# Optimization experiments

Hardware: AMD Instinct MI355X
Metric: run time of the kernel (lower is better)

## Reference

```python
import jax, jax.numpy as jnp
import numpy as np
from jax import lax

B, C, H, W = 8, 128, 96, 96
EXPAN = 4           # expan_att_chans
NUM_CHANS = 2
NUM_HEADS = NUM_CHANS * EXPAN          # 8
HEAD_DIM = C * EXPAN // NUM_HEADS      # 64
EPS = 1e-12  # F.normalize eps


def _gconv(x, w, b, groups):
    # torch Conv2d(kernel=3, padding=1, groups=groups), OIHW weight layout
    y = lax.conv_general_dilated(x, w, (1, 1), 'SAME',
                                 feature_group_count=groups,
                                 dimension_numbers=('NCHW', 'OIHW', 'NCHW'))
    return y + b[None, :, None, None]


def setup_inputs() -> dict:
    key = jax.random.key(0)
    k0, k1, k2 = jax.random.split(key, 3)
    x = jax.random.normal(k0, (B, C, H, W), jnp.float32)
    w_qkv = jax.random.normal(k1, (C * EXPAN * 3, 1, 3, 3), jnp.float32) * 0.05
    b_qkv = jnp.zeros((C * EXPAN * 3,), jnp.float32)
    t = jnp.ones((1, NUM_HEADS, 1, 1), jnp.float32)
    w_fus = jax.random.normal(k2, (C, EXPAN, 3, 3), jnp.float32) * 0.05
    b_fus = jnp.zeros((C,), jnp.float32)
    return {"x": x, "w_qkv": w_qkv, "b_qkv": b_qkv, "t": t,
            "w_fus": w_fus, "b_fus": b_fus}


def reference(x, w_qkv, b_qkv, t, w_fus, b_fus):
    # depthwise-grouped qkv conv: [B, C*EXPAN*3, H, W]
    qkv = _gconv(x, w_qkv, b_qkv, C)
    # view(B, C, 3e, H, W).transpose(1,2) -> [B, 3e, C, H, W]
    qkv = qkv.reshape(B, C, 3 * EXPAN, H, W).transpose(0, 2, 1, 3, 4)
    q, k, v = jnp.split(qkv, 3, axis=1)  # each [B, EXPAN, C, H, W]

    def heads(a):
        return a.reshape(B, NUM_HEADS, HEAD_DIM, H * W)

    q, k, v = heads(q), heads(k), heads(v)

    def l2n(a):
        return a / jnp.maximum(jnp.linalg.norm(a, axis=-1, keepdims=True), EPS)

    q, k = l2n(q), l2n(k)
    attn = jnp.einsum('bhdn,bhen->bhde', q, k) * t   # [B, nh, hd, hd]
    attn = jax.nn.softmax(attn, axis=-1)
    o = jnp.einsum('bhde,bhen->bhdn', attn, v)       # [B, nh, hd, HW]
    # view(B, EXPAN, C, H, W).transpose(1,2).flatten(1,2) -> [B, C*EXPAN, H, W]
    o = o.reshape(B, EXPAN, C, H, W).transpose(0, 2, 1, 3, 4).reshape(B, C * EXPAN, H, W)
    return _gconv(o, w_fus, b_fus, C)
```

## Files before the change

kernel.cpp:

```cpp
#include <hip/hip_runtime.h>
#include <hip/hip_bf16.h>
#include <stdint.h>

#define BB     8
#define CC     128
#define HW     9216
#define NHEAD  8
#define HD     64
#define NCH    16
#define CHUNK  576
#define KPAD   68
#define VTPAD  68

typedef __hip_bfloat16 bf16;
using frag16 = __attribute__((ext_vector_type(8))) short;
using f32x4  = __attribute__((ext_vector_type(4))) float;

__device__ __forceinline__ float b2f(bf16 v) { return __bfloat162float(v); }
__device__ __forceinline__ bf16  f2b(float v) { return __float2bfloat16(v); }

__device__ __forceinline__ float lo2f(unsigned int u) {
  union { unsigned int i; float f; } c; c.i = u << 16; return c.f;
}
__device__ __forceinline__ float hi2f(unsigned int u) {
  union { unsigned int i; float f; } c; c.i = u & 0xffff0000u; return c.f;
}

__device__ __forceinline__ unsigned int pack2(float a, float b) {
  union { __hip_bfloat162 h2; unsigned int u; } c;
  c.h2 = __float22bfloat162_rn(make_float2(a, b));
  return c.u;
}

__device__ __forceinline__ frag16 ldsfrag(const unsigned short* p) {
  uint2 lo = *(const uint2*)p;
  uint2 hi = *(const uint2*)(p + 4);
  union { unsigned int u[4]; frag16 f; } c;
  c.u[0] = lo.x; c.u[1] = lo.y; c.u[2] = hi.x; c.u[3] = hi.y;
  return c.f;
}
__device__ __forceinline__ void ldsst(unsigned short* p, uint4 v) {
  *(uint2*)p = make_uint2(v.x, v.y);
  *(uint2*)(p + 4) = make_uint2(v.z, v.w);
}

__device__ __forceinline__ void stage_plane(float* xs, const float* xp, int tid) {
  const float4 z4 = make_float4(0.f, 0.f, 0.f, 0.f);
  for (int i = tid; i < 98; i += 256) *(float4*)&xs[i * 100] = z4;
  for (int i = tid; i < 24; i += 256) *(float4*)&xs[4 + i * 4] = z4;
  for (int i = tid; i < 25; i += 256) *(float4*)&xs[9704 + i * 4] = z4;
  for (int i = tid; i < 96 * 24; i += 256) {
    int y = i / 24, g4 = i - y * 24;
    ((float4*)(xs + (y + 1) * 100 + 4))[g4] = ((const float4*)(xp + y * 96))[g4];
  }
}

__global__ __launch_bounds__(256) void k1_qkv(
    const float* __restrict__ x, const float* __restrict__ wq,
    const float* __restrict__ bq,
    bf16* __restrict__ qg, bf16* __restrict__ kg, bf16* __restrict__ vg,
    float* __restrict__ qn2, float* __restrict__ kn2, int b_base) {
  __shared__ float xs[98 * 100 + 4];
  __shared__ float red[32];
  int tid = threadIdx.x;
  int wave = tid >> 6, lane = tid & 63;
  int b = b_base + (blockIdx.x >> 7), c = blockIdx.x & 127;
  const float* xp = x + (size_t)(b * CC + c) * HW;
  stage_plane(xs, xp, tid);
  __syncthreads();

  int half = c >> 6, d = c & 63;
  int nidx[8];
  size_t basep[12];
#pragma unroll
  for (int j = 0; j < 12; ++j) {
    int e = j & 3;
    int h = e * 2 + half;
    int ni = (b * NHEAD + h) * HD + d;
    if (j < 8) nidx[j] = ni;
    basep[j] = (size_t)ni * HW;
  }
  const float* wrow = wq + c * 108;
  const float* brow = bq + c * 12;

  float ssq[8];
#pragma unroll
  for (int j = 0; j < 8; ++j) ssq[j] = 0.f;

#pragma unroll 1
  for (int it = 0; it < 5; ++it) {
    int u = it * 256 + tid;
    if (u < 1152) {
      int ly = u / 12;
      int x8 = (u - ly * 12) * 8;
      int p0 = ly * 96 + x8;
      float w10[3][10];
#pragma unroll
      for (int ky = 0; ky < 3; ++ky) {
        int basea = (ly + ky) * 100 + 4 + x8;
        float4 M0 = *(const float4*)&xs[basea];
        float4 M1 = *(const float4*)&xs[basea + 4];
        w10[ky][0] = xs[basea - 1];
        w10[ky][1] = M0.x; w10[ky][2] = M0.y; w10[ky][3] = M0.z; w10[ky][4] = M0.w;
        w10[ky][5] = M1.x; w10[ky][6] = M1.y; w10[ky][7] = M1.z; w10[ky][8] = M1.w;
        w10[ky][9] = xs[basea + 8];
      }
#pragma unroll
      for (int j = 0; j < 12; ++j) {
        float bias = brow[j];
        float a[8];
#pragma unroll
        for (int p = 0; p < 8; ++p) a[p] = bias;
#pragma unroll
        for (int ky = 0; ky < 3; ++ky)
#pragma unroll
          for (int kx = 0; kx < 3; ++kx) {
            float w = wrow[j * 9 + ky * 3 + kx];
#pragma unroll
            for (int p = 0; p < 8; ++p)
              a[p] = fmaf(w, w10[ky][kx + p], a[p]);
          }
        uint4 st;
        st.x = pack2(a[0], a[1]); st.y = pack2(a[2], a[3]);
        st.z = pack2(a[4], a[5]); st.w = pack2(a[6], a[7]);
        if (j < 4)      *(uint4*)(qg + basep[j] + p0) = st;
        else if (j < 8) *(uint4*)(kg + basep[j] + p0) = st;
        else            *(uint4*)(vg + basep[j] + p0) = st;
        if (j < 8) {
          float s2 = 0.f;
#pragma unroll
          for (int p = 0; p < 8; ++p) s2 = fmaf(a[p], a[p], s2);
          ssq[j] += s2;
        }
      }
    }
  }
#pragma unroll
  for (int j = 0; j < 8; ++j) {
    float v = ssq[j];
#pragma unroll
    for (int off = 32; off > 0; off >>= 1) v += __shfl_down(v, off);
    if (lane == 0) red[wave * 8 + j] = v;
  }
  __syncthreads();
  if (tid < 8) {
    float s = red[tid] + red[8 + tid] + red[16 + tid] + red[24 + tid];
    if (tid < 4) qn2[nidx[tid]] = s;
    else         kn2[nidx[tid]] = s;
  }
}

__global__ __launch_bounds__(256) void k2_gram(
    const bf16* __restrict__ qg, const bf16* __restrict__ kg,
    float* __restrict__ part) {
  __shared__ unsigned short sq[2][64 * KPAD];
  __shared__ unsigned short sk[2][64 * KPAD];
  int tid = threadIdx.x;
  int wave = tid >> 6;
  int lane = tid & 63;
  int chunk = blockIdx.x;
  int bh = blockIdx.y;
  const size_t base = (size_t)bh * HD * HW;
  int n0 = chunk * CHUNK;

  int srow = tid >> 3;
  int sseg = tid & 7;
  const bf16* qs0 = qg + base + (size_t)srow * HW + n0 + sseg * 8;
  const bf16* qs1 = qs0 + (size_t)32 * HW;
  const bf16* ks0 = kg + base + (size_t)srow * HW + n0 + sseg * 8;
  const bf16* ks1 = ks0 + (size_t)32 * HW;
  int d0 = srow * KPAD + sseg * 8;
  int d1 = (srow + 32) * KPAD + sseg * 8;

  int m = lane & 15;
  int k8 = lane >> 4;
  int arow = wave * 16 + m;

  f32x4 acc0 = {0.f, 0.f, 0.f, 0.f}, acc1 = acc0, acc2 = acc0, acc3 = acc0;

  uint4 rq0 = *(const uint4*)(qs0);
  uint4 rq1 = *(const uint4*)(qs1);
  uint4 rk0 = *(const uint4*)(ks0);
  uint4 rk1 = *(const uint4*)(ks1);
  ldsst(&sq[0][d0], rq0); ldsst(&sq[0][d1], rq1);
  ldsst(&sk[0][d0], rk0); ldsst(&sk[0][d1], rk1);
  __syncthreads();

#pragma unroll 1
  for (int s = 0; s < 9; ++s) {
    if (s < 8) {
      int off = (s + 1) * 64;
      rq0 = *(const uint4*)(qs0 + off);
      rq1 = *(const uint4*)(qs1 + off);
      rk0 = *(const uint4*)(ks0 + off);
      rk1 = *(const uint4*)(ks1 + off);
    }
    const unsigned short* sqc = sq[s & 1];
    const unsigned short* skc = sk[s & 1];
#pragma unroll
    for (int kk = 0; kk < 2; ++kk) {
      int co = kk * 32 + k8 * 8;
      frag16 a  = ldsfrag(&sqc[arow * KPAD + co]);
      frag16 b0 = ldsfrag(&skc[(m +  0) * KPAD + co]);
      frag16 b1 = ldsfrag(&skc[(m + 16) * KPAD + co]);
      frag16 b2 = ldsfrag(&skc[(m + 32) * KPAD + co]);
      frag16 b3 = ldsfrag(&skc[(m + 48) * KPAD + co]);
      acc0 = __builtin_amdgcn_mfma_f32_16x16x32_bf16(a, b0, acc0, 0, 0, 0);
      acc1 = __builtin_amdgcn_mfma_f32_16x16x32_bf16(a, b1, acc1, 0, 0, 0);
      acc2 = __builtin_amdgcn_mfma_f32_16x16x32_bf16(a, b2, acc2, 0, 0, 0);
      acc3 = __builtin_amdgcn_mfma_f32_16x16x32_bf16(a, b3, acc3, 0, 0, 0);
    }
    if (s < 8) {
      int nb = (s + 1) & 1;
      ldsst(&sq[nb][d0], rq0); ldsst(&sq[nb][d1], rq1);
      ldsst(&sk[nb][d0], rk0); ldsst(&sk[nb][d1], rk1);
      __syncthreads();
    }
  }

  float* po = part + (size_t)(bh * NCH + chunk) * 4096;
  int dr = wave * 16 + (lane >> 4) * 4;
  int e0 = lane & 15;
#pragma unroll
  for (int r = 0; r < 4; ++r) {
    po[(dr + r) * 64 +  0 + e0] = acc0[r];
    po[(dr + r) * 64 + 16 + e0] = acc1[r];
    po[(dr + r) * 64 + 32 + e0] = acc2[r];
    po[(dr + r) * 64 + 48 + e0] = acc3[r];
  }
}

__global__ __launch_bounds__(256) void k2_softmax(
    const float* __restrict__ part, bf16* __restrict__ ah, bf16* __restrict__ al,
    const float* __restrict__ qn2, const float* __restrict__ kn2,
    const float* __restrict__ t_f) {
  __shared__ float kns[64];
  int bh = blockIdx.x;
  int dq = blockIdx.y;
  int tid = threadIdx.x;
  if (tid < 64) kns[tid] = fmaxf(sqrtf(kn2[bh * 64 + tid]), 1e-12f);
  __syncthreads();
  int d  = dq * 16 + (tid >> 4);
  int e0 = (tid & 15) * 4;

  const float* pb = part + (size_t)bh * NCH * 4096 + d * 64 + e0;
  float4 s = make_float4(0.f, 0.f, 0.f, 0.f);
#pragma unroll
  for (int ch = 0; ch < NCH; ++ch) {
    float4 g = *(const float4*)&pb[ch * 4096];
    s.x += g.x; s.y += g.y; s.z += g.z; s.w += g.w;
  }
  float v[4] = {s.x, s.y, s.z, s.w};
  float sc = t_f[bh & 7] / fmaxf(sqrtf(qn2[bh * 64 + d]), 1e-12f);
  float m = -1e30f;
#pragma unroll
  for (int j = 0; j < 4; ++j) {
    v[j] = v[j] * sc / kns[e0 + j];
    m = fmaxf(m, v[j]);
  }
  m = fmaxf(m, __shfl_xor(m, 1));
  m = fmaxf(m, __shfl_xor(m, 2));
  m = fmaxf(m, __shfl_xor(m, 4));
  m = fmaxf(m, __shfl_xor(m, 8));
  float ssum = 0.f;
#pragma unroll
  for (int j = 0; j < 4; ++j) { v[j] = __expf(v[j] - m); ssum += v[j]; }
  ssum += __shfl_xor(ssum, 1);
  ssum += __shfl_xor(ssum, 2);
  ssum += __shfl_xor(ssum, 4);
  ssum += __shfl_xor(ssum, 8);
  float inv = 1.f / ssum;
  unsigned short hi16[4], lo16[4];
#pragma unroll
  for (int j = 0; j < 4; ++j) {
    float p = v[j] * inv;
    bf16 hi = f2b(p);
    float lo = p - b2f(hi);
    bf16 lov = f2b(lo);
    hi16[j] = *(unsigned short*)&hi;
    lo16[j] = *(unsigned short*)&lov;
  }
  const size_t base = (size_t)bh * 4096 + d * 64 + e0;
  *(ushort4*)(ah + base) = *(ushort4*)&hi16[0];
  *(ushort4*)(al + base) = *(ushort4*)&lo16[0];
}

__global__ __launch_bounds__(256) void k3_av(
    const bf16* __restrict__ ah, const bf16* __restrict__ al,
    const bf16* __restrict__ vg, bf16* __restrict__ og) {
  __shared__ unsigned short vt[256 * VTPAD];
  int tid = threadIdx.x;
  int wave = tid >> 6, lane = tid & 63;
  int chunk = blockIdx.x;
  int bh = blockIdx.y;
  int b = bh >> 3, h = bh & 7;
  int n0 = chunk * 256;
  int m = lane & 15;
  int k8 = (lane >> 4) * 8;
  int nwbase = wave * 64;

  const bf16* vp0 = vg + (size_t)bh * HD * HW + n0;
#pragma unroll
  for (int it = 0; it < 4; ++it) {
    int u = it * 256 + tid;
    int eq = u & 15, nq = u >> 4;
    const bf16* src = vp0 + (size_t)(eq * 4) * HW + nq * 4;
    ushort4 r0 = *(const ushort4*)(src);
    ushort4 r1 = *(const ushort4*)(src + HW);
    ushort4 r2 = *(const ushort4*)(src + 2 * HW);
    ushort4 r3 = *(const ushort4*)(src + (size_t)3 * HW);
    unsigned short* dst = &vt[(nq * 4) * VTPAD + eq * 4];
    *(ushort4*)(dst)             = make_ushort4(r0.x, r1.x, r2.x, r3.x);
    *(ushort4*)(dst + VTPAD)     = make_ushort4(r0.y, r1.y, r2.y, r3.y);
    *(ushort4*)(dst + 2 * VTPAD) = make_ushort4(r0.z, r1.z, r2.z, r3.z);
    *(ushort4*)(dst + 3 * VTPAD) = make_ushort4(r0.w, r1.w, r2.w, r3.w);
  }
  __syncthreads();

  const bf16* ahp = ah + (size_t)bh * 4096;
  const bf16* alp = al + (size_t)bh * 4096;

  f32x4 acc[4][4];
#pragma unroll
  for (int dt = 0; dt < 4; ++dt)
#pragma unroll
    for (int nt = 0; nt < 4; ++nt) acc[dt][nt] = {0.f, 0.f, 0.f, 0.f};

#pragma unroll
  for (int dt = 0; dt < 4; ++dt) {
    frag16 ahf[2], alf[2];
#pragma unroll
    for (int kh = 0; kh < 2; ++kh) {
      ahf[kh] = *(const frag16*)(ahp + (dt * 16 + m) * 64 + kh * 32 + k8);
      alf[kh] = *(const frag16*)(alp + (dt * 16 + m) * 64 + kh * 32 + k8);
    }
#pragma unroll
    for (int nt = 0; nt < 4; ++nt) {
      int nl = nwbase + nt * 16 + m;
#pragma unroll
      for (int kh = 0; kh < 2; ++kh) {
        frag16 bf = ldsfrag(&vt[nl * VTPAD + kh * 32 + k8]);
        acc[dt][nt] = __builtin_amdgcn_mfma_f32_16x16x32_bf16(ahf[kh], bf, acc[dt][nt], 0, 0, 0);
        acc[dt][nt] = __builtin_amdgcn_mfma_f32_16x16x32_bf16(alf[kh], bf, acc[dt][nt], 0, 0, 0);
      }
    }
  }

  int cc0 = (h & 1) * 256 + (h >> 1);
  bf16* ob = og + (size_t)b * 512 * HW;
  int q4 = (lane >> 4) * 4;
#pragma unroll
  for (int dt = 0; dt < 4; ++dt)
#pragma unroll
    for (int nt = 0; nt < 4; ++nt) {
      int n = n0 + nwbase + nt * 16 + m;
#pragma unroll
      for (int r = 0; r < 4; ++r) {
        int d = dt * 16 + q4 + r;
        ob[(size_t)(cc0 + d * 4) * HW + n] = f2b(acc[dt][nt][r]);
      }
    }
}

__global__ __launch_bounds__(256) void k4_fuse(
    const bf16* __restrict__ og, const float* __restrict__ wf,
    const float* __restrict__ bfu, float* __restrict__ out) {
  __shared__ unsigned short cells[26 * 100 * 4];
  int tid = threadIdx.x;
  int tile = blockIdx.x;
  int bc = blockIdx.y;
  int b = bc >> 7, c = bc & 127;
  int r0 = tile * 24 - 1;
  const uint2 z2 = make_uint2(0u, 0u);
  for (int i = tid; i < 52; i += 256) {
    int rr = i >> 1, cc = (i & 1) ? 98 : 1;
    *(uint2*)&cells[(rr * 100 + cc) * 4] = z2;
  }
  const uint4 z4 = make_uint4(0u, 0u, 0u, 0u);
  if (r0 < 0)
    for (int i = tid; i < 48; i += 256) *(uint4*)&cells[(0 * 100 + 2 + i * 2) * 4] = z4;
  if (r0 + 25 >= 96)
    for (int i = tid; i < 48; i += 256) *(uint4*)&cells[(25 * 100 + 2 + i * 2) * 4] = z4;
  const bf16* op = og + (size_t)(b * 512 + c * 4) * HW;
  for (int u = tid; u < 26 * 48; u += 256) {
    int rr = u / 48, pr = u - rr * 48;
    int gr = r0 + rr;
    if (gr >= 0 && gr < 96) {
      int gp = gr * 96 + pr * 2;
      unsigned int A = *(const unsigned int*)(op + gp);
      unsigned int B = *(const unsigned int*)(op + HW + gp);
      unsigned int C = *(const unsigned int*)(op + 2 * HW + gp);
      unsigned int D = *(const unsigned int*)(op + (size_t)3 * HW + gp);
      uint4 w;
      w.x = (A & 0xffffu) | (B << 16);
      w.y = (C & 0xffffu) | (D << 16);
      w.z = (A >> 16) | (B & 0xffff0000u);
      w.w = (C >> 16) | (D & 0xffff0000u);
      *(uint4*)&cells[(rr * 100 + 2 + pr * 2) * 4] = w;
    }
  }
  __syncthreads();
  const float* wrow = wf + c * 36;
  float bias = bfu[c];
  float* outp = out + (size_t)(b * CC + c) * HW + tile * 24 * 96;
#pragma unroll
  for (int pi = 0; pi < 9; ++pi) {
    int p = pi * 256 + tid;
    int ry = p / 96, x = p - ry * 96;
    float a0 = bias, a1 = 0.f, a2 = 0.f, a3 = 0.f;
#pragma unroll
    for (int ky = 0; ky < 3; ++ky) {
      int basec = (ry + ky) * 100 + 1 + x;
#pragma unroll
      for (int kx = 0; kx < 3; ++kx) {
        uint2 cc2 = *(const uint2*)&cells[(basec + kx) * 4];
        a0 = fmaf(wrow[0 + ky * 3 + kx],  lo2f(cc2.x), a0);
        a1 = fmaf(wrow[9 + ky * 3 + kx],  hi2f(cc2.x), a1);
        a2 = fmaf(wrow[18 + ky * 3 + kx], lo2f(cc2.y), a2);
        a3 = fmaf(wrow[27 + ky * 3 + kx], hi2f(cc2.y), a3);
      }
    }
    outp[p] = (a0 + a1) + (a2 + a3);
  }
}

extern "C" void kernel_launch(void* const* d_in, const int* in_sizes, int n_in,
                              void* d_out, int out_size, void* d_ws, size_t ws_size,
                              hipStream_t stream) {
  (void)in_sizes; (void)n_in; (void)out_size; (void)ws_size;
  const float* x   = (const float*)d_in[0];
  const float* wq  = (const float*)d_in[1];
  const float* bq  = (const float*)d_in[2];
  const float* tt  = (const float*)d_in[3];
  const float* wf  = (const float*)d_in[4];
  const float* bfu = (const float*)d_in[5];

  char* ws = (char*)d_ws;
  bf16*  qg    = (bf16*)(ws + 0);
  bf16*  kg    = (bf16*)(ws + 75497472);
  bf16*  vg    = (bf16*)(ws + 150994944);
  float* part  = (float*)(ws + 226492416);
  bf16*  ah    = (bf16*)(ws + 243269632);
  bf16*  al    = (bf16*)(ws + 243793920);
  float* qn2   = (float*)(ws + 244318208);
  float* kn2   = (float*)(ws + 244334592);
  bf16*  og    = qg;
  float* out   = (float*)d_out;

  hipLaunchKernelGGL(k1_qkv, dim3(512), dim3(256), 0, stream,
                     x, wq, bq, qg, kg, vg, qn2, kn2, 0);
  hipLaunchKernelGGL(k1_qkv, dim3(512), dim3(256), 0, stream,
                     x, wq, bq, qg, kg, vg, qn2, kn2, 4);
  hipLaunchKernelGGL(k2_gram, dim3(NCH, 64), dim3(256), 0, stream, qg, kg, part);
  hipLaunchKernelGGL(k2_softmax, dim3(64, 4), dim3(256), 0, stream,
                     part, ah, al, qn2, kn2, tt);
  hipLaunchKernelGGL(k3_av, dim3(36, 64), dim3(256), 0, stream, ah, al, vg, og);
  hipLaunchKernelGGL(k4_fuse, dim3(4, 1024), dim3(256), 0, stream, og, wf, bfu, out);
}
```

Before: 251.8 us.

## Double-chunk AV kernel with prefetched V, swapped MFMA operands, merged qkv launch

```diff
diff --git a/kernel.cpp b/kernel.cpp
--- a/kernel.cpp
+++ b/kernel.cpp
@@ -59,12 +59,12 @@
     const float* __restrict__ x, const float* __restrict__ wq,
     const float* __restrict__ bq,
     bf16* __restrict__ qg, bf16* __restrict__ kg, bf16* __restrict__ vg,
-    float* __restrict__ qn2, float* __restrict__ kn2, int b_base) {
+    float* __restrict__ qn2, float* __restrict__ kn2) {
   __shared__ float xs[98 * 100 + 4];
   __shared__ float red[32];
   int tid = threadIdx.x;
   int wave = tid >> 6, lane = tid & 63;
-  int b = b_base + (blockIdx.x >> 7), c = blockIdx.x & 127;
+  int b = blockIdx.x >> 7, c = blockIdx.x & 127;
   const float* xp = x + (size_t)(b * CC + c) * HW;
   stage_plane(xs, xp, tid);
   __syncthreads();
@@ -291,20 +291,34 @@
   __shared__ unsigned short vt[256 * VTPAD];
   int tid = threadIdx.x;
   int wave = tid >> 6, lane = tid & 63;
-  int chunk = blockIdx.x;
+  int cx = blockIdx.x;
   int bh = blockIdx.y;
   int b = bh >> 3, h = bh & 7;
-  int n0 = chunk * 256;
+  int n0 = cx * 512;
   int m = lane & 15;
   int k8 = (lane >> 4) * 8;
   int nwbase = wave * 64;
 
-  const bf16* vp0 = vg + (size_t)bh * HD * HW + n0;
+  const bf16* ahp = ah + (size_t)bh * 4096;
+  const bf16* alp = al + (size_t)bh * 4096;
+  frag16 b_hi[4][2], b_lo[4][2];
+#pragma unroll
+  for (int dt = 0; dt < 4; ++dt)
+#pragma unroll
+    for (int kh = 0; kh < 2; ++kh) {
+      b_hi[dt][kh] = *(const frag16*)(ahp + (dt * 16 + m) * 64 + kh * 32 + k8);
+      b_lo[dt][kh] = *(const frag16*)(alp + (dt * 16 + m) * 64 + kh * 32 + k8);
+    }
+
+  int ueq = tid & 15, unq = tid >> 4;
+  (void)ueq; (void)unq;
+  const bf16* vbase = vg + (size_t)bh * HD * HW;
+
 #pragma unroll
   for (int it = 0; it < 4; ++it) {
     int u = it * 256 + tid;
     int eq = u & 15, nq = u >> 4;
-    const bf16* src = vp0 + (size_t)(eq * 4) * HW + nq * 4;
+    const bf16* src = vbase + n0 + (size_t)(eq * 4) * HW + nq * 4;
     ushort4 r0 = *(const ushort4*)(src);
     ushort4 r1 = *(const ushort4*)(src + HW);
     ushort4 r2 = *(const ushort4*)(src + 2 * HW);
@@ -317,49 +331,71 @@
   }
   __syncthreads();
 
-  const bf16* ahp = ah + (size_t)bh * 4096;
-  const bf16* alp = al + (size_t)bh * 4096;
-
-  f32x4 acc[4][4];
-#pragma unroll
-  for (int dt = 0; dt < 4; ++dt)
-#pragma unroll
-    for (int nt = 0; nt < 4; ++nt) acc[dt][nt] = {0.f, 0.f, 0.f, 0.f};
-
-#pragma unroll
-  for (int dt = 0; dt < 4; ++dt) {
-    frag16 ahf[2], alf[2];
-#pragma unroll
-    for (int kh = 0; kh < 2; ++kh) {
-      ahf[kh] = *(const frag16*)(ahp + (dt * 16 + m) * 64 + kh * 32 + k8);
-      alf[kh] = *(const frag16*)(alp + (dt * 16 + m) * 64 + kh * 32 + k8);
-    }
-#pragma unroll
-    for (int nt = 0; nt < 4; ++nt) {
-      int nl = nwbase + nt * 16 + m;
-#pragma unroll
-      for (int kh = 0; kh < 2; ++kh) {
-        frag16 bf = ldsfrag(&vt[nl * VTPAD + kh * 32 + k8]);
-        acc[dt][nt] = __builtin_amdgcn_mfma_f32_16x16x32_bf16(ahf[kh], bf, acc[dt][nt], 0, 0, 0);
-        acc[dt][nt] = __builtin_amdgcn_mfma_f32_16x16x32_bf16(alf[kh], bf, acc[dt][nt], 0, 0, 0);
-      }
-    }
-  }
-
   int cc0 = (h & 1) * 256 + (h >> 1);
   bf16* ob = og + (size_t)b * 512 * HW;
   int q4 = (lane >> 4) * 4;
-#pragma unroll
-  for (int dt = 0; dt < 4; ++dt)
+
+  ushort4 pf[4][4];
+
+#pragma unroll 1
+  for (int s = 0; s < 2; ++s) {
+    if (s == 0) {
+#pragma unroll
+      for (int it = 0; it < 4; ++it) {
+        int u = it * 256 + tid;
+        int eq = u & 15, nq = u >> 4;
+        const bf16* src = vbase + n0 + 256 + (size_t)(eq * 4) * HW + nq * 4;
+        pf[it][0] = *(const ushort4*)(src);
+        pf[it][1] = *(const ushort4*)(src + HW);
+        pf[it][2] = *(const ushort4*)(src + 2 * HW);
+        pf[it][3] = *(const ushort4*)(src + (size_t)3 * HW);
+      }
+    }
+    f32x4 acc[4][4];
+#pragma unroll
+    for (int nt = 0; nt < 4; ++nt)
+#pragma unroll
+      for (int dt = 0; dt < 4; ++dt) acc[nt][dt] = {0.f, 0.f, 0.f, 0.f};
+
 #pragma unroll
     for (int nt = 0; nt < 4; ++nt) {
-      int n = n0 + nwbase + nt * 16 + m;
-#pragma unroll
-      for (int r = 0; r < 4; ++r) {
-        int d = dt * 16 + q4 + r;
-        ob[(size_t)(cc0 + d * 4) * HW + n] = f2b(acc[dt][nt][r]);
-      }
-    }
+      int nl = nwbase + nt * 16 + m;
+      frag16 af0 = ldsfrag(&vt[nl * VTPAD + 0 + k8]);
+      frag16 af1 = ldsfrag(&vt[nl * VTPAD + 32 + k8]);
+#pragma unroll
+      for (int dt = 0; dt < 4; ++dt) {
+        acc[nt][dt] = __builtin_amdgcn_mfma_f32_16x16x32_bf16(af0, b_hi[dt][0], acc[nt][dt], 0, 0, 0);
+        acc[nt][dt] = __builtin_amdgcn_mfma_f32_16x16x32_bf16(af0, b_lo[dt][0], acc[nt][dt], 0, 0, 0);
+        acc[nt][dt] = __builtin_amdgcn_mfma_f32_16x16x32_bf16(af1, b_hi[dt][1], acc[nt][dt], 0, 0, 0);
+        acc[nt][dt] = __builtin_amdgcn_mfma_f32_16x16x32_bf16(af1, b_lo[dt][1], acc[nt][dt], 0, 0, 0);
+      }
+    }
+    int ns0 = n0 + s * 256 + nwbase + q4;
+#pragma unroll
+    for (int nt = 0; nt < 4; ++nt)
+#pragma unroll
+      for (int dt = 0; dt < 4; ++dt) {
+        int d = dt * 16 + m;
+        uint2 st = make_uint2(pack2(acc[nt][dt][0], acc[nt][dt][1]),
+                              pack2(acc[nt][dt][2], acc[nt][dt][3]));
+        *(uint2*)(ob + (size_t)(cc0 + d * 4) * HW + ns0 + nt * 16) = st;
+      }
+    if (s == 0) {
+      __syncthreads();
+#pragma unroll
+      for (int it = 0; it < 4; ++it) {
+        int u = it * 256 + tid;
+        int eq = u & 15, nq = u >> 4;
+        unsigned short* dst = &vt[(nq * 4) * VTPAD + eq * 4];
+        ushort4 r0 = pf[it][0], r1 = pf[it][1], r2 = pf[it][2], r3 = pf[it][3];
+        *(ushort4*)(dst)             = make_ushort4(r0.x, r1.x, r2.x, r3.x);
+        *(ushort4*)(dst + VTPAD)     = make_ushort4(r0.y, r1.y, r2.y, r3.y);
+        *(ushort4*)(dst + 2 * VTPAD) = make_ushort4(r0.z, r1.z, r2.z, r3.z);
+        *(ushort4*)(dst + 3 * VTPAD) = make_ushort4(r0.w, r1.w, r2.w, r3.w);
+      }
+      __syncthreads();
+    }
+  }
 }
 
 __global__ __launch_bounds__(256) void k4_fuse(
@@ -447,13 +483,11 @@
   bf16*  og    = qg;
   float* out   = (float*)d_out;
 
-  hipLaunchKernelGGL(k1_qkv, dim3(512), dim3(256), 0, stream,
-                     x, wq, bq, qg, kg, vg, qn2, kn2, 0);
-  hipLaunchKernelGGL(k1_qkv, dim3(512), dim3(256), 0, stream,
-                     x, wq, bq, qg, kg, vg, qn2, kn2, 4);
+  hipLaunchKernelGGL(k1_qkv, dim3(1024), dim3(256), 0, stream,
+                     x, wq, bq, qg, kg, vg, qn2, kn2);
   hipLaunchKernelGGL(k2_gram, dim3(NCH, 64), dim3(256), 0, stream, qg, kg, part);
   hipLaunchKernelGGL(k2_softmax, dim3(64, 4), dim3(256), 0, stream,
                      part, ah, al, qn2, kn2, tt);
-  hipLaunchKernelGGL(k3_av, dim3(36, 64), dim3(256), 0, stream, ah, al, vg, og);
+  hipLaunchKernelGGL(k3_av, dim3(18, 64), dim3(256), 0, stream, ah, al, vg, og);
   hipLaunchKernelGGL(k4_fuse, dim3(4, 1024), dim3(256), 0, stream, og, wf, bfu, out);
 }
```

Result: faster. 239.2 us (-5.0%).
